# Kernel optimization log

Measured on AMD Instinct MI355X. Metric: run time of the kernel, lower is better.

## Reference

```python
import jax, jax.numpy as jnp
import numpy as np

B, S, D, H = 32, 2048, 1024, 1024

def setup_inputs() -> dict:
    key = jax.random.key(0)
    k1, k2, k3, k4, k5 = jax.random.split(key, 5)
    return {
        "query": jax.random.normal(k1, (B, D), dtype=jnp.float32),
        "values": jax.random.normal(k2, (B, S, D), dtype=jnp.float32),
        "W1": jax.random.normal(k3, (D, H), dtype=jnp.float32) / np.sqrt(D),
        "W2": jax.random.normal(k4, (D, H), dtype=jnp.float32) / np.sqrt(D),
        "v": jax.random.uniform(k5, (H,), dtype=jnp.float32),
    }

def reference(query, values, W1, W2, v):
    # query: [B, D], values: [B, S, D]
    query_proj = query @ W2                              # [B, H]
    keys_proj = jnp.einsum('bsd,dh->bsh', values, W1)     # [B, S, H]
    energy = jnp.tanh(query_proj[:, None, :] + keys_proj) # [B, S, H]
    scores = jnp.einsum('bsh,h->bs', energy, v)           # [B, S]
    attention_weights = jax.nn.softmax(scores, axis=-1)   # [B, S]
    context = jnp.einsum('bs,bsd->bd', attention_weights, values)  # [B, D]
    return context, attention_weights
```

## Files before the change

### kernel.cpp

```cpp
#include <hip/hip_runtime.h>
#include <hip/hip_fp16.h>


typedef _Float16 v8h  __attribute__((ext_vector_type(8)));
typedef __fp16   v2hf __attribute__((ext_vector_type(2)));
typedef float    v4f  __attribute__((ext_vector_type(4)));

#define B_DIM 32
#define S_DIM 2048
#define D_DIM 1024
#define H_DIM 1024

#define WS_W1T    0u
#define WS_QP     2097152u
#define WS_SCORES (WS_QP + 131072u)

__device__ __forceinline__ void gl_lds16(const _Float16* g, _Float16* l) {
    __builtin_amdgcn_global_load_lds(
        (const __attribute__((address_space(1))) void*)g,
        (__attribute__((address_space(3))) void*)l, 16, 0, 0);
}

__global__ void k_prep(const float* __restrict__ W1, _Float16* __restrict__ w1t,
                       const float* __restrict__ query, const float* __restrict__ W2,
                       float* __restrict__ qp, float* __restrict__ scores) {
    __shared__ float smem[64 * 65];
    int bid = blockIdx.x, tid = threadIdx.x;
    if (bid < 256) {
        int b = bid >> 3, hc = bid & 7;
        #pragma unroll
        for (int i = 0; i < 4; ++i)
            smem[i * 256 + tid] = query[b * D_DIM + i * 256 + tid];
        __syncthreads();
        int hh = tid & 127, half = tid >> 7;
        int h = hc * 128 + hh;
        const float* w2p = W2 + (size_t)(half * 512) * H_DIM + h;
        float acc = 0.f;
        #pragma unroll 8
        for (int d = 0; d < 512; ++d)
            acc += smem[half * 512 + d] * w2p[(size_t)d * H_DIM];
        smem[1024 + tid] = acc;
        __syncthreads();
        if (tid < 128)
            qp[b * H_DIM + hc * 128 + tid] = smem[1024 + tid] + smem[1024 + 128 + tid];
    } else if (bid < 512) {
        int j = bid - 256;
        int h0 = (j & 15) * 64, d0 = (j >> 4) * 64;
        #pragma unroll
        for (int i = 0; i < 16; ++i) {
            int idx = i * 256 + tid;
            int dd = idx >> 6, hh = idx & 63;
            smem[dd * 65 + hh] = W1[(size_t)(d0 + dd) * H_DIM + h0 + hh];
        }
        __syncthreads();
        #pragma unroll
        for (int i = 0; i < 16; ++i) {
            int idx = i * 256 + tid;
            int hh = idx >> 6, dd = idx & 63;
            w1t[(size_t)(h0 + hh) * D_DIM + d0 + dd] = (_Float16)smem[dd * 65 + hh];
        }
    } else {
        int j = bid - 512;
        size_t o = (size_t)j * 2048 + tid * 8;
        *(v4f*)(scores + o)     = (v4f){0.f, 0.f, 0.f, 0.f};
        *(v4f*)(scores + o + 4) = (v4f){0.f, 0.f, 0.f, 0.f};
    }
}

__global__ __launch_bounds__(512, 2) void k_scores(
        const float* __restrict__ values, const _Float16* __restrict__ w1t,
        const float* __restrict__ qp, const float* __restrict__ v,
        float* __restrict__ scores) {
    __shared__ _Float16 As[2][256 * 64];
    __shared__ _Float16 Bs[2][256 * 64];

    int tid = threadIdx.x;
    int wid = tid >> 6, lane = tid & 63;
    int quad = lane >> 4, l15 = lane & 15;
    int wm = wid >> 2, wn = wid & 3;

    int bid = blockIdx.x;
    int idx = (bid & 7) * 128 + (bid >> 3);
    int np  = idx & 3;
    int mtb = idx >> 2;
    int b   = mtb >> 3;
    int m0  = (mtb & 7) * 256;
    int n0  = np * 256;

    int arow  = tid >> 3;
    int aslot = tid & 7;
    const float* abase = values + ((size_t)b * S_DIM + m0) * D_DIM;
    int a_row[4], a_off[4];
    #pragma unroll
    for (int i = 0; i < 4; ++i) {
        int row  = i * 64 + arow;
        a_row[i] = row;
        a_off[i] = row * 64 + (aslot ^ (row & 7)) * 8;
    }

    int srow = lane >> 3;
    int kg   = lane & 7;

    v4f acc[8][4];
    #pragma unroll
    for (int i = 0; i < 8; ++i)
        #pragma unroll
        for (int j = 0; j < 4; ++j) acc[i][j] = (v4f){0.f, 0.f, 0.f, 0.f};

    v4f ap[8];

    #pragma unroll
    for (int i = 0; i < 4; ++i) {
        const float* p = abase + (size_t)a_row[i] * D_DIM + aslot * 8;
        ap[2 * i]     = *(const v4f*)p;
        ap[2 * i + 1] = *(const v4f*)(p + 4);
    }
    #pragma unroll
    for (int i = 0; i < 4; ++i) {
        union { v8h h; v2hf p[4]; } u;
        u.p[0] = __builtin_amdgcn_cvt_pkrtz(ap[2 * i][0], ap[2 * i][1]);
        u.p[1] = __builtin_amdgcn_cvt_pkrtz(ap[2 * i][2], ap[2 * i][3]);
        u.p[2] = __builtin_amdgcn_cvt_pkrtz(ap[2 * i + 1][0], ap[2 * i + 1][1]);
        u.p[3] = __builtin_amdgcn_cvt_pkrtz(ap[2 * i + 1][2], ap[2 * i + 1][3]);
        *(v8h*)(&As[0][a_off[i]]) = u.h;
    }
    #pragma unroll
    for (int i = 0; i < 4; ++i) {
        int brow = i * 64 + wid * 8;
        int row  = brow + srow;
        int kgs  = kg ^ (row & 7);
        gl_lds16(w1t + (size_t)(n0 + row) * D_DIM + kgs * 8, &Bs[0][brow * 64]);
    }
    #pragma unroll
    for (int i = 0; i < 4; ++i) {
        const float* p = abase + (size_t)a_row[i] * D_DIM + 64 + aslot * 8;
        ap[2 * i]     = *(const v4f*)p;
        ap[2 * i + 1] = *(const v4f*)(p + 4);
    }
    asm volatile("s_waitcnt vmcnt(8) lgkmcnt(0)" ::: "memory");
    __builtin_amdgcn_s_barrier();

    for (int kt = 0; kt < 16; ++kt) {
        int cur = kt & 1;
        if (kt < 15) {
            #pragma unroll
            for (int i = 0; i < 4; ++i) {
                union { v8h h; v2hf p[4]; } u;
                u.p[0] = __builtin_amdgcn_cvt_pkrtz(ap[2 * i][0], ap[2 * i][1]);
                u.p[1] = __builtin_amdgcn_cvt_pkrtz(ap[2 * i][2], ap[2 * i][3]);
                u.p[2] = __builtin_amdgcn_cvt_pkrtz(ap[2 * i + 1][0], ap[2 * i + 1][1]);
                u.p[3] = __builtin_amdgcn_cvt_pkrtz(ap[2 * i + 1][2], ap[2 * i + 1][3]);
                *(v8h*)(&As[cur ^ 1][a_off[i]]) = u.h;
            }
            int k1 = (kt + 1) * 64;
            #pragma unroll
            for (int i = 0; i < 4; ++i) {
                int brow = i * 64 + wid * 8;
                int row  = brow + srow;
                int kgs  = kg ^ (row & 7);
                gl_lds16(w1t + (size_t)(n0 + row) * D_DIM + k1 + kgs * 8,
                         &Bs[cur ^ 1][brow * 64]);
            }
            int k2 = ((kt + 2) & 15) * 64;
            #pragma unroll
            for (int i = 0; i < 4; ++i) {
                const float* p = abase + (size_t)a_row[i] * D_DIM + k2 + aslot * 8;
                ap[2 * i]     = *(const v4f*)p;
                ap[2 * i + 1] = *(const v4f*)(p + 4);
            }
            __builtin_amdgcn_sched_barrier(0);
        }

        __builtin_amdgcn_s_setprio(1);
        #pragma unroll
        for (int kk = 0; kk < 2; ++kk) {
            v8h af[8], bf[4];
            #pragma unroll
            for (int mt = 0; mt < 8; ++mt) {
                int row = wm * 128 + mt * 16 + l15;
                int ph  = (kk * 4 + quad) ^ (row & 7);
                af[mt] = *(const v8h*)(&As[cur][row * 64 + ph * 8]);
            }
            #pragma unroll
            for (int nt = 0; nt < 4; ++nt) {
                int row = wn * 64 + nt * 16 + l15;
                int ph  = (kk * 4 + quad) ^ (row & 7);
                bf[nt] = *(const v8h*)(&Bs[cur][row * 64 + ph * 8]);
            }
            #pragma unroll
            for (int mt = 0; mt < 8; ++mt)
                #pragma unroll
                for (int nt = 0; nt < 4; ++nt)
                    acc[mt][nt] = __builtin_amdgcn_mfma_f32_16x16x32_f16(
                        af[mt], bf[nt], acc[mt][nt], 0, 0, 0);
        }
        __builtin_amdgcn_s_setprio(0);

        asm volatile("s_waitcnt vmcnt(8) lgkmcnt(0)" ::: "memory");
        __builtin_amdgcn_s_barrier();
    }

    float qpv[4], vv[4];
    #pragma unroll
    for (int nt = 0; nt < 4; ++nt) {
        int ng = n0 + wn * 64 + nt * 16 + l15;
        qpv[nt] = qp[b * H_DIM + ng];
        vv[nt]  = v[ng];
    }

    float* s_scores = (float*)&As[0][0];
    if (tid < 256) s_scores[tid] = 0.f;
    __syncthreads();

    #pragma unroll
    for (int mt = 0; mt < 8; ++mt) {
        #pragma unroll
        for (int r = 0; r < 4; ++r) {
            float s = 0.f;
            #pragma unroll
            for (int nt = 0; nt < 4; ++nt) {
                float x = acc[mt][nt][r] + qpv[nt];
                float e = __expf(2.f * x);
                s += (1.f - 2.f / (e + 1.f)) * vv[nt];
            }
            s += __shfl_xor(s, 1);
            s += __shfl_xor(s, 2);
            s += __shfl_xor(s, 4);
            s += __shfl_xor(s, 8);
            if (l15 == 0)
                atomicAdd(&s_scores[wm * 128 + mt * 16 + quad * 4 + r], s);
        }
    }
    __syncthreads();
    if (tid < 256) atomicAdd(&scores[(size_t)b * S_DIM + m0 + tid], s_scores[tid]);
}

__global__ __launch_bounds__(1024) void k_finish(
        const float* __restrict__ scores, const float* __restrict__ values,
        float* __restrict__ wout, float* __restrict__ ctx) {
    __shared__ float s_w[2048];
    __shared__ int   s_idx[2048];
    __shared__ float red[16];
    __shared__ float s_bcast;
    __shared__ int   s_cnt;

    int b = blockIdx.x, tid = threadIdx.x;
    int lane = tid & 63, wid = tid >> 6;

    float s0 = scores[b * S_DIM + tid];
    float s1 = scores[b * S_DIM + 1024 + tid];

    float m = fmaxf(s0, s1);
    #pragma unroll
    for (int off = 1; off <= 32; off <<= 1) m = fmaxf(m, __shfl_xor(m, off));
    if (lane == 0) red[wid] = m;
    if (tid == 0) s_cnt = 0;
    __syncthreads();
    if (tid == 0) {
        float mm = red[0];
        #pragma unroll
        for (int i = 1; i < 16; ++i) mm = fmaxf(mm, red[i]);
        s_bcast = mm;
    }
    __syncthreads();
    float rowmax = s_bcast;

    float e0 = __expf(s0 - rowmax);
    float e1 = __expf(s1 - rowmax);
    float sum = e0 + e1;
    #pragma unroll
    for (int off = 1; off <= 32; off <<= 1) sum += __shfl_xor(sum, off);
    if (lane == 0) red[wid] = sum;
    __syncthreads();
    if (tid == 0) {
        float ss = red[0];
        #pragma unroll
        for (int i = 1; i < 16; ++i) ss += red[i];
        s_bcast = 1.f / ss;
    }
    __syncthreads();
    float inv = s_bcast;

    float w0 = e0 * inv, w1 = e1 * inv;
    wout[b * S_DIM + tid]        = w0;
    wout[b * S_DIM + 1024 + tid] = w1;
    s_w[tid]        = w0;
    s_w[tid + 1024] = w1;

    if (w0 > 1e-7f) { int p = atomicAdd(&s_cnt, 1); s_idx[p] = tid; }
    if (w1 > 1e-7f) { int p = atomicAdd(&s_cnt, 1); s_idx[p] = tid + 1024; }
    __syncthreads();
    int cnt = s_cnt;

    float acc = 0.f;
    const float* vb = values + (size_t)b * S_DIM * D_DIM + tid;
    for (int i = 0; i < cnt; ++i) {
        int s = s_idx[i];
        acc += s_w[s] * vb[(size_t)s * D_DIM];
    }
    ctx[b * D_DIM + tid] = acc;
}

extern "C" void kernel_launch(void* const* d_in, const int* in_sizes, int n_in,
                              void* d_out, int out_size, void* d_ws, size_t ws_size,
                              hipStream_t stream) {
    const float* query  = (const float*)d_in[0];
    const float* values = (const float*)d_in[1];
    const float* W1     = (const float*)d_in[2];
    const float* W2     = (const float*)d_in[3];
    const float* v      = (const float*)d_in[4];

    char* ws = (char*)d_ws;
    _Float16* w1t = (_Float16*)(ws + WS_W1T);
    float* qp     = (float*)(ws + WS_QP);
    float* scores = (float*)(ws + WS_SCORES);

    float* ctx  = (float*)d_out;
    float* wout = (float*)d_out + 32768;

    k_prep<<<dim3(544), 256, 0, stream>>>(W1, w1t, query, W2, qp, scores);
    k_scores<<<dim3(1024), 512, 0, stream>>>(values, w1t, qp, v, scores);
    k_finish<<<dim3(32), 1024, 0, stream>>>(scores, values, wout, ctx);
}
```

Measured before the change: 591.6 us.

## Pre-convert values to fp16 in prep kernel and stream both GEMM operands via LDS DMA

Adds a prep pass that converts the whole fp32 values tensor to an fp16 workspace copy. The scores GEMM then loads both A and B tiles with global_load_lds directly into LDS, which removes the per-thread register loads, packed conversions and LDS stores. The main loop is restructured into a gemm_step helper that splits the MFMA work into halves with barriers and issues the next-tile prefetch in between. The cost is an extra full read of values (256MB) plus a 128MB fp16 write, in exchange for halving the values traffic in the GEMM, which reads each values tile four times across the N tiles.

New measurement: 556.9 us. 5.9% less time.

```diff
diff --git a/kernel.cpp b/kernel.cpp
--- a/kernel.cpp
+++ b/kernel.cpp
@@ -3,7 +3,6 @@
 
 
 typedef _Float16 v8h  __attribute__((ext_vector_type(8)));
-typedef __fp16   v2hf __attribute__((ext_vector_type(2)));
 typedef float    v4f  __attribute__((ext_vector_type(4)));
 
 #define B_DIM 32
@@ -11,8 +10,9 @@
 #define D_DIM 1024
 #define H_DIM 1024
 
-#define WS_W1T    0u
-#define WS_QP     2097152u
+#define WS_V16    0u
+#define WS_W1T    134217728u
+#define WS_QP     (WS_W1T + 2097152u)
 #define WS_SCORES (WS_QP + 131072u)
 
 __device__ __forceinline__ void gl_lds16(const _Float16* g, _Float16* l) {
@@ -21,12 +21,23 @@
         (__attribute__((address_space(3))) void*)l, 16, 0, 0);
 }
 
-__global__ void k_prep(const float* __restrict__ W1, _Float16* __restrict__ w1t,
+__global__ void k_prep(const float* __restrict__ values, _Float16* __restrict__ v16,
+                       const float* __restrict__ W1, _Float16* __restrict__ w1t,
                        const float* __restrict__ query, const float* __restrict__ W2,
                        float* __restrict__ qp, float* __restrict__ scores) {
     __shared__ float smem[64 * 65];
     int bid = blockIdx.x, tid = threadIdx.x;
-    if (bid < 256) {
+    if (bid >= 544) {
+        size_t i = ((size_t)(bid - 544) * 256 + tid) * 8;
+        v4f f0 = __builtin_nontemporal_load((const v4f*)(values + i));
+        v4f f1 = __builtin_nontemporal_load((const v4f*)(values + i + 4));
+        v8h hv;
+        hv[0] = (_Float16)f0[0]; hv[1] = (_Float16)f0[1];
+        hv[2] = (_Float16)f0[2]; hv[3] = (_Float16)f0[3];
+        hv[4] = (_Float16)f1[0]; hv[5] = (_Float16)f1[1];
+        hv[6] = (_Float16)f1[2]; hv[7] = (_Float16)f1[3];
+        *(v8h*)(v16 + i) = hv;
+    } else if (bid < 256) {
         int b = bid >> 3, hc = bid & 7;
         #pragma unroll
         for (int i = 0; i < 4; ++i)
@@ -67,8 +78,65 @@
     }
 }
 
+
+template<bool PF>
+__device__ __forceinline__ void gemm_step(
+        const _Float16* CA, const _Float16* CB,
+        _Float16* NA, _Float16* NB,
+        const _Float16* a16, const _Float16* bw, int k1,
+        int wm, int wn, int quad, int l15, int wid, int srow, int kg,
+        v4f acc[8][4]) {
+    #pragma unroll
+    for (int kk = 0; kk < 2; ++kk) {
+        v8h bf[4];
+        #pragma unroll
+        for (int j = 0; j < 4; ++j) {
+            int row = wn * 64 + j * 16 + l15;
+            int ph  = (kk * 4 + quad) ^ (row & 7);
+            bf[j] = *(const v8h*)(&CB[row * 64 + ph * 8]);
+        }
+        #pragma unroll
+        for (int mh = 0; mh < 2; ++mh) {
+            v8h af[4];
+            #pragma unroll
+            for (int i = 0; i < 4; ++i) {
+                int row = wm * 128 + mh * 64 + i * 16 + l15;
+                int ph  = (kk * 4 + quad) ^ (row & 7);
+                af[i] = *(const v8h*)(&CA[row * 64 + ph * 8]);
+            }
+            if (PF && kk == 0) {
+                #pragma unroll
+                for (int i = 0; i < 4; ++i) {
+                    int brow = i * 64 + wid * 8;
+                    int row  = brow + srow;
+                    int kgs  = kg ^ (row & 7);
+                    if (mh == 0)
+                        gl_lds16(a16 + (size_t)row * D_DIM + k1 + kgs * 8,
+                                 &NA[brow * 64]);
+                    else
+                        gl_lds16(bw + (size_t)row * D_DIM + k1 + kgs * 8,
+                                 &NB[brow * 64]);
+                }
+            }
+            __builtin_amdgcn_s_barrier();
+            asm volatile("s_waitcnt lgkmcnt(0)" ::: "memory");
+            __builtin_amdgcn_sched_barrier(0);
+            __builtin_amdgcn_s_setprio(1);
+            #pragma unroll
+            for (int i = 0; i < 4; ++i)
+                #pragma unroll
+                for (int j = 0; j < 4; ++j)
+                    acc[mh * 4 + i][j] = __builtin_amdgcn_mfma_f32_16x16x32_f16(
+                        af[i], bf[j], acc[mh * 4 + i][j], 0, 0, 0);
+            __builtin_amdgcn_s_setprio(0);
+        }
+    }
+    if (PF) asm volatile("s_waitcnt vmcnt(0)" ::: "memory");
+    __builtin_amdgcn_s_barrier();
+}
+
 __global__ __launch_bounds__(512, 2) void k_scores(
-        const float* __restrict__ values, const _Float16* __restrict__ w1t,
+        const _Float16* __restrict__ v16, const _Float16* __restrict__ w1t,
         const float* __restrict__ qp, const float* __restrict__ v,
         float* __restrict__ scores) {
     __shared__ _Float16 As[2][256 * 64];
@@ -87,19 +155,10 @@
     int m0  = (mtb & 7) * 256;
     int n0  = np * 256;
 
-    int arow  = tid >> 3;
-    int aslot = tid & 7;
-    const float* abase = values + ((size_t)b * S_DIM + m0) * D_DIM;
-    int a_row[4], a_off[4];
-    #pragma unroll
-    for (int i = 0; i < 4; ++i) {
-        int row  = i * 64 + arow;
-        a_row[i] = row;
-        a_off[i] = row * 64 + (aslot ^ (row & 7)) * 8;
-    }
-
     int srow = lane >> 3;
     int kg   = lane & 7;
+    const _Float16* a16 = v16 + ((size_t)b * S_DIM + m0) * D_DIM;
+    const _Float16* bw  = w1t + (size_t)n0 * D_DIM;
 
     v4f acc[8][4];
     #pragma unroll
@@ -107,98 +166,25 @@
         #pragma unroll
         for (int j = 0; j < 4; ++j) acc[i][j] = (v4f){0.f, 0.f, 0.f, 0.f};
 
-    v4f ap[8];
-
-    #pragma unroll
-    for (int i = 0; i < 4; ++i) {
-        const float* p = abase + (size_t)a_row[i] * D_DIM + aslot * 8;
-        ap[2 * i]     = *(const v4f*)p;
-        ap[2 * i + 1] = *(const v4f*)(p + 4);
-    }
-    #pragma unroll
-    for (int i = 0; i < 4; ++i) {
-        union { v8h h; v2hf p[4]; } u;
-        u.p[0] = __builtin_amdgcn_cvt_pkrtz(ap[2 * i][0], ap[2 * i][1]);
-        u.p[1] = __builtin_amdgcn_cvt_pkrtz(ap[2 * i][2], ap[2 * i][3]);
-        u.p[2] = __builtin_amdgcn_cvt_pkrtz(ap[2 * i + 1][0], ap[2 * i + 1][1]);
-        u.p[3] = __builtin_amdgcn_cvt_pkrtz(ap[2 * i + 1][2], ap[2 * i + 1][3]);
-        *(v8h*)(&As[0][a_off[i]]) = u.h;
-    }
     #pragma unroll
     for (int i = 0; i < 4; ++i) {
         int brow = i * 64 + wid * 8;
         int row  = brow + srow;
         int kgs  = kg ^ (row & 7);
-        gl_lds16(w1t + (size_t)(n0 + row) * D_DIM + kgs * 8, &Bs[0][brow * 64]);
-    }
-    #pragma unroll
-    for (int i = 0; i < 4; ++i) {
-        const float* p = abase + (size_t)a_row[i] * D_DIM + 64 + aslot * 8;
-        ap[2 * i]     = *(const v4f*)p;
-        ap[2 * i + 1] = *(const v4f*)(p + 4);
-    }
-    asm volatile("s_waitcnt vmcnt(8) lgkmcnt(0)" ::: "memory");
+        gl_lds16(a16 + (size_t)row * D_DIM + kgs * 8, &As[0][brow * 64]);
+        gl_lds16(bw  + (size_t)row * D_DIM + kgs * 8, &Bs[0][brow * 64]);
+    }
+    asm volatile("s_waitcnt vmcnt(0)" ::: "memory");
     __builtin_amdgcn_s_barrier();
 
-    for (int kt = 0; kt < 16; ++kt) {
-        int cur = kt & 1;
-        if (kt < 15) {
-            #pragma unroll
-            for (int i = 0; i < 4; ++i) {
-                union { v8h h; v2hf p[4]; } u;
-                u.p[0] = __builtin_amdgcn_cvt_pkrtz(ap[2 * i][0], ap[2 * i][1]);
-                u.p[1] = __builtin_amdgcn_cvt_pkrtz(ap[2 * i][2], ap[2 * i][3]);
-                u.p[2] = __builtin_amdgcn_cvt_pkrtz(ap[2 * i + 1][0], ap[2 * i + 1][1]);
-                u.p[3] = __builtin_amdgcn_cvt_pkrtz(ap[2 * i + 1][2], ap[2 * i + 1][3]);
-                *(v8h*)(&As[cur ^ 1][a_off[i]]) = u.h;
-            }
-            int k1 = (kt + 1) * 64;
-            #pragma unroll
-            for (int i = 0; i < 4; ++i) {
-                int brow = i * 64 + wid * 8;
-                int row  = brow + srow;
-                int kgs  = kg ^ (row & 7);
-                gl_lds16(w1t + (size_t)(n0 + row) * D_DIM + k1 + kgs * 8,
-                         &Bs[cur ^ 1][brow * 64]);
-            }
-            int k2 = ((kt + 2) & 15) * 64;
-            #pragma unroll
-            for (int i = 0; i < 4; ++i) {
-                const float* p = abase + (size_t)a_row[i] * D_DIM + k2 + aslot * 8;
-                ap[2 * i]     = *(const v4f*)p;
-                ap[2 * i + 1] = *(const v4f*)(p + 4);
-            }
-            __builtin_amdgcn_sched_barrier(0);
-        }
-
-        __builtin_amdgcn_s_setprio(1);
-        #pragma unroll
-        for (int kk = 0; kk < 2; ++kk) {
-            v8h af[8], bf[4];
-            #pragma unroll
-            for (int mt = 0; mt < 8; ++mt) {
-                int row = wm * 128 + mt * 16 + l15;
-                int ph  = (kk * 4 + quad) ^ (row & 7);
-                af[mt] = *(const v8h*)(&As[cur][row * 64 + ph * 8]);
-            }
-            #pragma unroll
-            for (int nt = 0; nt < 4; ++nt) {
-                int row = wn * 64 + nt * 16 + l15;
-                int ph  = (kk * 4 + quad) ^ (row & 7);
-                bf[nt] = *(const v8h*)(&Bs[cur][row * 64 + ph * 8]);
-            }
-            #pragma unroll
-            for (int mt = 0; mt < 8; ++mt)
-                #pragma unroll
-                for (int nt = 0; nt < 4; ++nt)
-                    acc[mt][nt] = __builtin_amdgcn_mfma_f32_16x16x32_f16(
-                        af[mt], bf[nt], acc[mt][nt], 0, 0, 0);
-        }
-        __builtin_amdgcn_s_setprio(0);
-
-        asm volatile("s_waitcnt vmcnt(8) lgkmcnt(0)" ::: "memory");
-        __builtin_amdgcn_s_barrier();
-    }
+    for (int t = 0; t < 15; ++t) {
+        int cur = t & 1;
+        gemm_step<true>(As[cur], Bs[cur], As[cur ^ 1], Bs[cur ^ 1],
+                        a16, bw, (t + 1) * 64,
+                        wm, wn, quad, l15, wid, srow, kg, acc);
+    }
+    gemm_step<false>(As[1], Bs[1], As[0], Bs[0], a16, bw, 0,
+                     wm, wn, quad, l15, wid, srow, kg, acc);
 
     float qpv[4], vv[4];
     #pragma unroll
@@ -311,6 +297,7 @@
     const float* v      = (const float*)d_in[4];
 
     char* ws = (char*)d_ws;
+    _Float16* v16 = (_Float16*)(ws + WS_V16);
     _Float16* w1t = (_Float16*)(ws + WS_W1T);
     float* qp     = (float*)(ws + WS_QP);
     float* scores = (float*)(ws + WS_SCORES);
@@ -318,7 +305,7 @@
     float* ctx  = (float*)d_out;
     float* wout = (float*)d_out + 32768;
 
-    k_prep<<<dim3(544), 256, 0, stream>>>(W1, w1t, query, W2, qp, scores);
-    k_scores<<<dim3(1024), 512, 0, stream>>>(values, w1t, qp, v, scores);
+    k_prep<<<dim3(33312), 256, 0, stream>>>(values, v16, W1, w1t, query, W2, qp, scores);
+    k_scores<<<dim3(1024), 512, 0, stream>>>(v16, w1t, qp, v, scores);
     k_finish<<<dim3(32), 1024, 0, stream>>>(scores, values, wout, ctx);
 }
```
